# Kernel tuning notes

Measured on AMD Instinct MI355X. Metric: run time of the kernel, lower is better.

The kernel has to match this reference:

```python
import jax, jax.numpy as jnp
import numpy as np

B, T, V, LMAX = 32, 1024, 1024, 128
BLANK = 0
NEG = jnp.float32(-1e30)


def setup_inputs() -> dict:
    key = jax.random.key(0)
    k1, k2, k3, k4 = jax.random.split(key, 4)
    ys_hat = jax.random.normal(k1, (B, T, V), dtype=jnp.float32)
    ys_pad = jax.random.randint(k2, (B, LMAX), 1, V, dtype=jnp.int32)  # no blanks in labels
    hlens = jax.random.randint(k3, (B,), T // 2, T + 1, dtype=jnp.int32)
    ys_lens = jax.random.randint(k4, (B,), LMAX // 2, LMAX + 1, dtype=jnp.int32)
    return {"ys_hat": ys_hat, "ys_pad": ys_pad, "hlens": hlens, "ys_lens": ys_lens}


def _ctc_neg_log_lik(log_probs, ys_pad, hlens, ys_lens):
    # log_probs: [B, T, V] log-softmaxed frame activations
    b, t, v = log_probs.shape
    lmax = ys_pad.shape[1]
    s = 2 * lmax + 1  # extended label length (blanks interleaved)
    # extended labels: blank, y1, blank, y2, ..., blank
    ext = jnp.full((b, s), BLANK, dtype=ys_pad.dtype).at[:, 1::2].set(ys_pad)  # [B, S]
    # gather per-frame log-probs of extended labels -> [B, T, S]
    lp_ext = jnp.take_along_axis(log_probs, jnp.broadcast_to(ext[:, None, :], (b, t, s)), axis=2)
    # skip transition allowed at s if ext[s] != blank and ext[s] != ext[s-2]
    ext_m2 = jnp.pad(ext[:, :-2], ((0, 0), (2, 0)), constant_values=BLANK)
    skip = (jnp.arange(s)[None, :] >= 2) & (ext != BLANK) & (ext != ext_m2)  # [B, S]

    def shift(a, n):
        return jnp.pad(a[:, :-n], ((0, 0), (n, 0)), constant_values=NEG)

    # t = 0: paths can start at s=0 (blank) or s=1 (first label)
    alpha0 = jnp.full((b, s), NEG, dtype=log_probs.dtype)
    alpha0 = alpha0.at[:, 0].set(lp_ext[:, 0, 0]).at[:, 1].set(lp_ext[:, 0, 1])

    def step(alpha, inp):
        tt, lp_t = inp  # lp_t: [B, S]
        cand = jnp.logaddexp(alpha, shift(alpha, 1))
        cand = jnp.logaddexp(cand, jnp.where(skip, shift(alpha, 2), NEG))
        new = cand + lp_t
        alpha = jnp.where((tt < hlens)[:, None], new, alpha)  # freeze past each hlen
        return alpha, None

    ts = jnp.arange(1, t)
    alpha, _ = jax.lax.scan(step, alpha0, (ts, jnp.swapaxes(lp_ext, 0, 1)[1:]))

    # terminal states: s = 2*ys_len (final blank) or 2*ys_len - 1 (last label)
    i1 = (2 * ys_lens)[:, None]
    i2 = (2 * ys_lens - 1)[:, None]
    a1 = jnp.take_along_axis(alpha, i1, axis=1)[:, 0]
    a2 = jnp.take_along_axis(alpha, i2, axis=1)[:, 0]
    return -jnp.logaddexp(a1, a2)  # [B]


def reference(ys_hat, ys_pad, hlens, ys_lens):
    # log_softmax over vocab, then CTC forward DP; reduction='sum' then / B
    log_probs = jax.nn.log_softmax(ys_hat, axis=-1)
    losses = _ctc_neg_log_lik(log_probs, ys_pad, hlens, ys_lens)
    return jnp.sum(losses) / ys_hat.shape[0]
```

## Files before the change

kernel.cpp:

```cpp
#include <hip/hip_runtime.h>
#include <math.h>

#define BB    32
#define TT    1024
#define VV    1024
#define LM    128
#define SS    257
#define SP    272
#define RNORM 16
#define PF    16
#define RPW   8

__global__ __launch_bounds__(256) void ctc_row_kernel(
    const float* __restrict__ ys_hat, const int* __restrict__ ys_pad,
    const int* __restrict__ hlens, float* __restrict__ lp)
{
    __shared__ float srow[4][VV];
    const int w    = threadIdx.x >> 6;
    const int lane = threadIdx.x & 63;
    const int gw   = blockIdx.x * 4 + w;
    const int b    = gw >> 7;
    const int t0   = (gw & 127) * RPW;
    const int hl   = hlens[b];
    int nrows = hl - t0;
    if (nrows <= 0) return;
    if (nrows > RPW) nrows = RPW;

    const int lab0 = ys_pad[b * LM + 2 * lane];
    const int lab1 = ys_pad[b * LM + 2 * lane + 1];
    const float* xr  = ys_hat + ((size_t)b * TT + t0) * VV;
    float*       lpo = lp     + ((size_t)b * TT + t0) * SP;

    float4 va0, va1, va2, va3, vb0, vb1, vb2, vb3;
    {
        const float4* cx = (const float4*)xr;
        va0 = cx[lane]; va1 = cx[lane + 64]; va2 = cx[lane + 128]; va3 = cx[lane + 192];
    }

#define ROW_STEP(C0, C1, C2, C3, N0, N1, N2, N3)                               \
    {                                                                          \
        if (i + 1 < nrows) {   \
            const float4* nx = (const float4*)(xr + (size_t)(i + 1) * VV);     \
            N0 = nx[lane]; N1 = nx[lane + 64];                                 \
            N2 = nx[lane + 128]; N3 = nx[lane + 192];                          \
        }                                                                      \
        float4* sw = (float4*)srow[w];                                         \
        sw[lane] = C0; sw[lane + 64] = C1;                                     \
        sw[lane + 128] = C2; sw[lane + 192] = C3;                              \
        float m = fmaxf(fmaxf(fmaxf(C0.x, C0.y), fmaxf(C0.z, C0.w)),          \
                        fmaxf(fmaxf(C1.x, C1.y), fmaxf(C1.z, C1.w)));          \
        m = fmaxf(m, fmaxf(fmaxf(fmaxf(C2.x, C2.y), fmaxf(C2.z, C2.w)),       \
                           fmaxf(fmaxf(C3.x, C3.y), fmaxf(C3.z, C3.w))));      \
        float s = __expf(C0.x - m) + __expf(C0.y - m) + __expf(C0.z - m) +     \
                  __expf(C0.w - m) + __expf(C1.x - m) + __expf(C1.y - m) +     \
                  __expf(C1.z - m) + __expf(C1.w - m) + __expf(C2.x - m) +     \
                  __expf(C2.y - m) + __expf(C2.z - m) + __expf(C2.w - m) +     \
                  __expf(C3.x - m) + __expf(C3.y - m) + __expf(C3.z - m) +     \
                  __expf(C3.w - m);                                            \
        _Pragma("unroll")                                                      \
        for (int off = 32; off; off >>= 1) {      \
            const float mo = __shfl_xor(m, off);                               \
            const float so = __shfl_xor(s, off);                               \
            const float mn = fmaxf(m, mo);                                     \
            s = s * __expf(m - mn) + so * __expf(mo - mn);                     \
            m = mn;                                                            \
        }                                                                      \
        const float xbv = srow[w][0];                                          \
        const float x1v = srow[w][lab0];                                       \
        const float x3v = srow[w][lab1];                                       \
        const float pb  = __expf(xbv - m);                                     \
        ((float4*)(lpo + (size_t)i * SP))[lane] =                              \
            make_float4(pb, __expf(x1v - m), pb, __expf(x3v - m));             \
        if (lane < 16) {               \
            float val = 0.f;                                                   \
            if (lane == 0) val = pb;                    \
            if (lane == 1) val = __logf(s);                      \
            lpo[(size_t)i * SP + 256 + lane] = val;                            \
        }                                                                      \
    }

    int i = 0;
    for (;;) {
        ROW_STEP(va0, va1, va2, va3, vb0, vb1, vb2, vb3)
        if (++i >= nrows) break;
        ROW_STEP(vb0, vb1, vb2, vb3, va0, va1, va2, va3)
        if (++i >= nrows) break;
    }
#undef ROW_STEP
}

#define DPP_ADDF(x, ctrl)                                                       \
    x = x + __int_as_float(__builtin_amdgcn_update_dpp(                         \
            0, __float_as_int(x), ctrl, 0xf, 0xf, true))
#define DPP_IMAX(x, ctrl)                                                       \
    {                                                                           \
        const int _o = __builtin_amdgcn_update_dpp(0, x, ctrl, 0xf, 0xf, true); \
        x = (x > _o) ? x : _o;                                                  \
    }
#define RLANEF(x, l) __int_as_float(__builtin_amdgcn_readlane(__float_as_int(x), (l)))
#define RLANEI(x, l) __builtin_amdgcn_readlane((x), (l))

__device__ __forceinline__ double dpp_wave_shr1_f64(double x)
{
    const int lo = __builtin_amdgcn_update_dpp(
        0, __double2loint(x), 0x138, 0xf, 0xf, true);
    const int hi = __builtin_amdgcn_update_dpp(
        0, __double2hiint(x), 0x138, 0xf, 0xf, true);
    return __hiloint2double(hi, lo);
}

__global__ __launch_bounds__(64, 1) void ctc_dp_kernel(
    const float* __restrict__ lp_all, const int* __restrict__ ys_pad,
    const int* __restrict__ hlens, const int* __restrict__ ys_lens,
    float* __restrict__ out)
{
    __shared__ double sh[SS];
    const int b    = blockIdx.x;
    const int lane = threadIdx.x;
    const int hl   = hlens[b];
    const float* lp = lp_all + (size_t)b * TT * SP;

    float sv[16];
#pragma unroll
    for (int jj = 0; jj < 16; ++jj)
        sv[jj] = lp[(size_t)(lane + jj * 64) * SP + 257];

    float4 qr[PF];
#pragma unroll
    for (int j = 0; j < PF; ++j)
        qr[j] = ((const float4*)(lp + (size_t)(1 + j) * SP))[lane];

    const int* lab = ys_pad + b * LM;
    const double sk1d = (lane > 0 && lab[2 * lane] != lab[2 * lane - 1]) ? 1.0 : 0.0;
    const double sk3d = (lab[2 * lane + 1] != lab[2 * lane]) ? 1.0 : 0.0;

    float ssv = 0.f;
#pragma unroll
    for (int jj = 0; jj < 16; ++jj)
        ssv += (lane + jj * 64 < hl) ? sv[jj] : 0.f;
    DPP_ADDF(ssv, 0x111); DPP_ADDF(ssv, 0x112); DPP_ADDF(ssv, 0x114); DPP_ADDF(ssv, 0x118);
    const float ssw = RLANEF(ssv, 15) + RLANEF(ssv, 31) + RLANEF(ssv, 47) + RLANEF(ssv, 63);

    const float4 q0 = ((const float4*)lp)[lane];
    double a0 = (lane == 0) ? (double)q0.x : 0.0;
    double a1 = (lane == 0) ? (double)q0.y : 0.0;
    double a2 = 0.0, a3 = 0.0, a4 = 0.0;
    int ksum = 0;

#define RENORM_BODY                                                            \
    {                                                                          \
        double m = fmax(fmax(fmax(a0, a1), fmax(a2, a3)), a4);                 \
        m = fmax(m, 1e-300);                          \
        int hi = __double2hiint(m);            \
        DPP_IMAX(hi, 0x111); DPP_IMAX(hi, 0x112);                              \
        DPP_IMAX(hi, 0x114); DPP_IMAX(hi, 0x118);                              \
        const int h0 = RLANEI(hi, 15), h1 = RLANEI(hi, 31);                    \
        const int h2 = RLANEI(hi, 47), h3 = RLANEI(hi, 63);                    \
        int hw = (h0 > h1) ? h0 : h1;                                          \
        hw = (hw > h2) ? hw : h2;                                              \
        hw = (hw > h3) ? hw : h3;                                              \
        const int k = (hw >> 20) - 1022;             \
        const double sc = __hiloint2double((1023 - k) << 20, 0);  \
        ksum += k;                           \
        a0 *= sc; a1 *= sc; a2 *= sc; a3 *= sc; a4 *= sc;                      \
    }

#define DP_STEP(q)                                                             \
    {                                                                          \
        const double qx = (double)(q).x;                                       \
        const double qy = (double)(q).y;                                       \
        const double qw = (double)(q).w;       \
        const double n1 = dpp_wave_shr1_f64(a3);   \
        const double c0 = (a0 + n1) * qx;                                      \
        const double c1 = fma(sk1d, n1, a0 + a1) * qy;                         \
        const double c2 = (a2 + a1) * qx;                                      \
        const double c3 = (a3 + fma(sk3d, a1, a2)) * qw;                       \
        const double c4 = (a4 + a3) * qx;    \
        a0 = c0; a1 = c1; a2 = c2; a3 = c3; a4 = c4;                           \
    }

    int t0 = 1;
    for (; t0 + 2 * PF - 1 <= hl - 1; t0 += PF) {
        const float* pfp = lp + (size_t)(t0 + PF) * SP;
#pragma unroll
        for (int j = 0; j < PF; ++j) {
            const float4 q = qr[j];
            qr[j] = ((const float4*)(pfp + (size_t)j * SP))[lane];
            if (j == PF - 1) RENORM_BODY
            DP_STEP(q)
        }
    }
    for (; t0 < hl; t0 += PF) {
#pragma unroll
        for (int j = 0; j < PF; ++j) {
            const int t = t0 + j;
            const float4 q = qr[j];
            int tp = t + PF; if (tp > hl - 1) tp = hl - 1;
            qr[j] = ((const float4*)(lp + (size_t)tp * SP))[lane];
            if (t < hl) {
                if ((t & (RNORM - 1)) == 0) RENORM_BODY
                DP_STEP(q)
            }
        }
    }
#undef DP_STEP
#undef RENORM_BODY

    sh[4 * lane]     = a0;
    sh[4 * lane + 1] = a1;
    sh[4 * lane + 2] = a2;
    sh[4 * lane + 3] = a3;
    if (lane == 63) sh[256] = a4;
    __syncthreads();
    if (lane == 0) {
        const int L = ys_lens[b];
        const double aL = sh[2 * L] + sh[2 * L - 1];
        const double loss = (double)ssw -
            (log(aL) + (double)ksum * 0.6931471805599453);
        atomicAdd(out, (float)(loss * (1.0 / (double)BB)));
    }
}

extern "C" void kernel_launch(void* const* d_in, const int* in_sizes, int n_in,
                              void* d_out, int out_size, void* d_ws, size_t ws_size,
                              hipStream_t stream) {
    const float* ys_hat  = (const float*)d_in[0];
    const int*   ys_pad  = (const int*)d_in[1];
    const int*   hlens   = (const int*)d_in[2];
    const int*   ys_lens = (const int*)d_in[3];
    float* out = (float*)d_out;

    float* lp_raw = (float*)d_ws;

    hipMemsetAsync(d_out, 0, sizeof(float), stream);

    ctc_row_kernel<<<BB * TT / (4 * RPW), 256, 0, stream>>>(ys_hat, ys_pad, hlens, lp_raw);
    ctc_dp_kernel<<<BB, 64, 0, stream>>>(lp_raw, ys_pad, hlens, ys_lens, out);
}
```

Before: 252.0 us.

## Normalize CTC probabilities by blank emission and drop the output memset

Each frame's emission probabilities are rescaled by the blank probability, so blank states need no multiply in the DP and only two floats per lane are stored and loaded instead of four. The per-frame log correction (log-sum plus max minus blank logit) is written once and summed into the loss. Output zeroing moves from a separate memset into the row kernel, removing one stream operation. The rescaling changes the DP's numeric ranges, though the existing renormalisation should cover this.

New measurement: 251.8 us. Within noise of the previous version (-0.1%).

```diff
diff --git a/kernel.cpp b/kernel.cpp
--- a/kernel.cpp
+++ b/kernel.cpp
@@ -13,9 +13,11 @@
 
 __global__ __launch_bounds__(256) void ctc_row_kernel(
     const float* __restrict__ ys_hat, const int* __restrict__ ys_pad,
-    const int* __restrict__ hlens, float* __restrict__ lp)
+    const int* __restrict__ hlens, float* __restrict__ lp,
+    float* __restrict__ out)
 {
     __shared__ float srow[4][VV];
+    if (blockIdx.x == 0 && threadIdx.x == 0) *out = 0.f;
     const int w    = threadIdx.x >> 6;
     const int lane = threadIdx.x & 63;
     const int gw   = blockIdx.x * 4 + w;
@@ -68,13 +70,11 @@
         const float xbv = srow[w][0];                                          \
         const float x1v = srow[w][lab0];                                       \
         const float x3v = srow[w][lab1];                                       \
-        const float pb  = __expf(xbv - m);                                     \
-        ((float4*)(lpo + (size_t)i * SP))[lane] =                              \
-            make_float4(pb, __expf(x1v - m), pb, __expf(x3v - m));             \
+        ((float2*)(lpo + (size_t)i * SP))[lane] =                              \
+            make_float2(__expf(x1v - xbv), __expf(x3v - xbv));                 \
         if (lane < 16) {               \
             float val = 0.f;                                                   \
-            if (lane == 0) val = pb;                    \
-            if (lane == 1) val = __logf(s);                      \
+            if (lane == 0) val = __logf(s) + (m - xbv);     \
             lpo[(size_t)i * SP + 256 + lane] = val;                            \
         }                                                                      \
     }
@@ -123,12 +123,12 @@
     float sv[16];
 #pragma unroll
     for (int jj = 0; jj < 16; ++jj)
-        sv[jj] = lp[(size_t)(lane + jj * 64) * SP + 257];
-
-    float4 qr[PF];
+        sv[jj] = lp[(size_t)(lane + jj * 64) * SP + 256];
+
+    float2 qr[PF];
 #pragma unroll
     for (int j = 0; j < PF; ++j)
-        qr[j] = ((const float4*)(lp + (size_t)(1 + j) * SP))[lane];
+        qr[j] = ((const float2*)(lp + (size_t)(1 + j) * SP))[lane];
 
     const int* lab = ys_pad + b * LM;
     const double sk1d = (lane > 0 && lab[2 * lane] != lab[2 * lane - 1]) ? 1.0 : 0.0;
@@ -141,9 +141,9 @@
     DPP_ADDF(ssv, 0x111); DPP_ADDF(ssv, 0x112); DPP_ADDF(ssv, 0x114); DPP_ADDF(ssv, 0x118);
     const float ssw = RLANEF(ssv, 15) + RLANEF(ssv, 31) + RLANEF(ssv, 47) + RLANEF(ssv, 63);
 
-    const float4 q0 = ((const float4*)lp)[lane];
-    double a0 = (lane == 0) ? (double)q0.x : 0.0;
-    double a1 = (lane == 0) ? (double)q0.y : 0.0;
+    const float2 q0 = ((const float2*)lp)[lane];
+    double a0 = (lane == 0) ? 1.0 : 0.0;
+    double a1 = (lane == 0) ? (double)q0.x : 0.0;
     double a2 = 0.0, a3 = 0.0, a4 = 0.0;
     int ksum = 0;
 
@@ -167,15 +167,14 @@
 
 #define DP_STEP(q)                                                             \
     {                                                                          \
-        const double qx = (double)(q).x;                                       \
-        const double qy = (double)(q).y;                                       \
-        const double qw = (double)(q).w;       \
+        const double ry = (double)(q).x;            \
+        const double rw = (double)(q).y;            \
         const double n1 = dpp_wave_shr1_f64(a3);   \
-        const double c0 = (a0 + n1) * qx;                                      \
-        const double c1 = fma(sk1d, n1, a0 + a1) * qy;                         \
-        const double c2 = (a2 + a1) * qx;                                      \
-        const double c3 = (a3 + fma(sk3d, a1, a2)) * qw;                       \
-        const double c4 = (a4 + a3) * qx;    \
+        const double c0 = a0 + n1;                          \
+        const double c1 = fma(sk1d, n1, a0 + a1) * ry;                         \
+        const double c2 = a2 + a1;                          \
+        const double c3 = (a3 + fma(sk3d, a1, a2)) * rw;                       \
+        const double c4 = a4 + a3;              \
         a0 = c0; a1 = c1; a2 = c2; a3 = c3; a4 = c4;                           \
     }
 
@@ -184,8 +183,8 @@
         const float* pfp = lp + (size_t)(t0 + PF) * SP;
 #pragma unroll
         for (int j = 0; j < PF; ++j) {
-            const float4 q = qr[j];
-            qr[j] = ((const float4*)(pfp + (size_t)j * SP))[lane];
+            const float2 q = qr[j];
+            qr[j] = ((const float2*)(pfp + (size_t)j * SP))[lane];
             if (j == PF - 1) RENORM_BODY
             DP_STEP(q)
         }
@@ -194,9 +193,9 @@
 #pragma unroll
         for (int j = 0; j < PF; ++j) {
             const int t = t0 + j;
-            const float4 q = qr[j];
+            const float2 q = qr[j];
             int tp = t + PF; if (tp > hl - 1) tp = hl - 1;
-            qr[j] = ((const float4*)(lp + (size_t)tp * SP))[lane];
+            qr[j] = ((const float2*)(lp + (size_t)tp * SP))[lane];
             if (t < hl) {
                 if ((t & (RNORM - 1)) == 0) RENORM_BODY
                 DP_STEP(q)
@@ -232,8 +231,6 @@
 
     float* lp_raw = (float*)d_ws;
 
-    hipMemsetAsync(d_out, 0, sizeof(float), stream);
-
-    ctc_row_kernel<<<BB * TT / (4 * RPW), 256, 0, stream>>>(ys_hat, ys_pad, hlens, lp_raw);
+    ctc_row_kernel<<<BB * TT / (4 * RPW), 256, 0, stream>>>(ys_hat, ys_pad, hlens, lp_raw, out);
     ctc_dp_kernel<<<BB, 64, 0, stream>>>(lp_raw, ys_pad, hlens, ys_lens, out);
 }
```
